# Performance work log

Hardware: AMD Instinct MI355X
Metric: run time of the kernel (lower is better)

## Reference

```python
import jax, jax.numpy as jnp
import numpy as np

HEAD = 12
HEAD_DIM = 64  # dim // head = 768 // 12


def setup_inputs() -> dict:
    key = jax.random.key(0)
    k1, k2, k3 = jax.random.split(key, 3)
    B, N, D = 4, 2048, 768
    scale = 1.0 / np.sqrt(D)
    return {
        "x": jax.random.normal(k1, (B, N, D), dtype=jnp.float32),
        "w_qkv": jax.random.normal(k2, (D, 3 * D), dtype=jnp.float32) * scale,
        "w_proj": jax.random.normal(k3, (D, D), dtype=jnp.float32) * scale,
        "b_proj": jnp.zeros((D,), dtype=jnp.float32),
    }


def reference(x, w_qkv, w_proj, b_proj):
    B, N, D = x.shape
    qkv = x @ w_qkv  # [B, N, 3D]
    q, k, v = jnp.split(qkv, 3, axis=-1)
    # [B, H, N, k]
    def heads(t):
        return t.reshape(B, N, HEAD, HEAD_DIM).transpose(0, 2, 1, 3)
    q, k, v = heads(q), heads(k), heads(v)
    attn = jnp.einsum("bhnd,bhmd->bhnm", q, k) / jnp.sqrt(jnp.float32(HEAD_DIM))
    attn_prob = jax.nn.softmax(attn, axis=-1)  # dropout p=0.0 -> identity
    out = jnp.einsum("bhnm,bhmd->bhnd", attn_prob, v)
    out = out.transpose(0, 2, 1, 3).reshape(B, N, D)
    return out @ w_proj + b_proj
```

## Files before the change

### kernel.cpp

```cpp
#include <hip/hip_runtime.h>

typedef unsigned short u16;
typedef unsigned int u32;
typedef u16 u16x4 __attribute__((ext_vector_type(4)));
typedef u16 u16x8 __attribute__((ext_vector_type(8)));
typedef u32 u32x2 __attribute__((ext_vector_type(2)));
typedef u32 u32x4 __attribute__((ext_vector_type(4)));
typedef __bf16 bf16x8 __attribute__((ext_vector_type(8)));
typedef float f32x4 __attribute__((ext_vector_type(4)));
typedef float f32x16 __attribute__((ext_vector_type(16)));

#define MFMA16 __builtin_amdgcn_mfma_f32_16x16x32_bf16
#define MFMA32 __builtin_amdgcn_mfma_f32_32x32x16_bf16

__device__ __forceinline__ u16 f2bf(float f) {
  return __builtin_bit_cast(u16, (__bf16)f);
}

__device__ __forceinline__ u32 pk2bf(float a, float b) {
  return (u32)__builtin_bit_cast(u16, (__bf16)a) |
         ((u32)__builtin_bit_cast(u16, (__bf16)b) << 16);
}

__device__ __forceinline__ u32x2 swap32(u32 a, u32 b, int hi) {
#if __has_builtin(__builtin_amdgcn_permlane32_swap)
  (void)hi;
  return __builtin_amdgcn_permlane32_swap(a, b, false, false);
#else
  u32 sa = (u32)__shfl_xor((int)a, 32), sb = (u32)__shfl_xor((int)b, 32);
  u32x2 r;
  r[0] = hi ? sb : a;
  r[1] = hi ? b : sa;
  return r;
#endif
}

__device__ __forceinline__ void gload_lds16(const void* g, void* l) {
  __builtin_amdgcn_global_load_lds(
      (const __attribute__((address_space(1))) u32*)g,
      (__attribute__((address_space(3))) u32*)l, 16, 0, 0);
}

__global__ __launch_bounds__(256)
void prepass_kernel(const float* __restrict__ x, u16* __restrict__ xb,
                    const float* __restrict__ wq, u16* __restrict__ wqT,
                    const float* __restrict__ wp, u16* __restrict__ wpT) {
  __shared__ float t[32][33];
  const int bid = blockIdx.x, tid = threadIdx.x;
  if (bid < 6144) {
    const int i = bid * 256 + tid;
    float4 v = reinterpret_cast<const float4*>(x)[i];
    u16x4 o;
    o[0] = f2bf(v.x); o[1] = f2bf(v.y); o[2] = f2bf(v.z); o[3] = f2bf(v.w);
    reinterpret_cast<u16x4*>(xb)[i] = o;
    return;
  }
  const float* w;
  u16* wt;
  int N, b2;
  if (bid < 7872) { b2 = bid - 6144; w = wq; wt = wqT; N = 2304; }
  else            { b2 = bid - 7872; w = wp; wt = wpT; N = 768; }
  const int K = 768;
  const int bk = (b2 % 24) * 32, bn = (b2 / 24) * 32;
  const int xx = tid & 31, yy = tid >> 5;
#pragma unroll
  for (int j = 0; j < 32; j += 8)
    t[yy + j][xx] = w[(size_t)(bk + yy + j) * N + bn + xx];
  __syncthreads();
#pragma unroll
  for (int j = 0; j < 32; j += 8)
    wt[(size_t)(bn + yy + j) * K + bk + xx] = f2bf(t[xx][yy + j]);
}

#define QSCALE 0.18033688011112042f

template <int NTOT, int EPI, int NT>
__global__ __launch_bounds__(256)
void gemm_bf16_kernel(const u16* __restrict__ A, const u16* __restrict__ BT,
                      u16* __restrict__ qo, u16* __restrict__ ko,
                      u16* __restrict__ vt, float* __restrict__ outF,
                      const float* __restrict__ bias) {
  __shared__ u16 sh[16384];
  u16* As = sh;
  u16* Bs = sh + 8192;
  const int tid = threadIdx.x;
  const int l = tid & 63, w = tid >> 6;
  const int lr = l & 15, lg = l >> 4;
  const int swz = (blockIdx.x & 7) * (8 * NT) + (blockIdx.x >> 3);
  const int mtile = swz / NT;
  const int ntile = swz % NT;
  const int mbase = mtile * 128, nbase = ntile * 128;
  const int wr = (w >> 1) * 64, wc = (w & 1) * 64;

  f32x4 acc[4][4] = {};

  for (int k0 = 0; k0 < 768; k0 += 64) {
#pragma unroll
    for (int i = 0; i < 4; ++i) {
      const int c = w * 64 + i * 256 + l;
      const int row = c >> 3, c16 = c & 7;
      const int sc = c16 ^ (row & 7);
      gload_lds16(A + (size_t)(mbase + row) * 768 + k0 + sc * 8,
                  &As[(size_t)(w * 64 + i * 256) * 8]);
      gload_lds16(BT + (size_t)(nbase + row) * 768 + k0 + sc * 8,
                  &Bs[(size_t)(w * 64 + i * 256) * 8]);
    }
    __syncthreads();
#pragma unroll
    for (int ks = 0; ks < 2; ++ks) {
      bf16x8 af[4], bfr[4];
#pragma unroll
      for (int m = 0; m < 4; ++m) {
        const int row = wr + m * 16 + lr;
        const int byte = (row * 128 + ks * 64 + lg * 16) ^ ((row & 7) << 4);
        af[m] = *reinterpret_cast<const bf16x8*>((const char*)As + byte);
      }
#pragma unroll
      for (int n = 0; n < 4; ++n) {
        const int row = wc + n * 16 + lr;
        const int byte = (row * 128 + ks * 64 + lg * 16) ^ ((row & 7) << 4);
        bfr[n] = *reinterpret_cast<const bf16x8*>((const char*)Bs + byte);
      }
#pragma unroll
      for (int m = 0; m < 4; ++m)
#pragma unroll
        for (int n = 0; n < 4; ++n)
          acc[m][n] = MFMA16(af[m], bfr[n], acc[m][n], 0, 0, 0);
    }
    __syncthreads();
  }

  if (EPI == 0 && ntile >= 12) {
    u16* vts = sh;
#pragma unroll
    for (int m = 0; m < 4; ++m)
#pragma unroll
      for (int n = 0; n < 4; ++n)
#pragma unroll
        for (int r = 0; r < 4; ++r) {
          const int col = wc + n * 16 + lr;
          const int row = wr + m * 16 + lg * 4 + r;
          const int byte = col * 256 + ((row * 2) ^ ((col & 7) << 4));
          *reinterpret_cast<u16*>((char*)vts + byte) = f2bf(acc[m][n][r]);
        }
    __syncthreads();
    const int b2 = mbase >> 11, nn0 = mbase & 2047;
#pragma unroll
    for (int i = 0; i < 8; ++i) {
      const int idx = i * 256 + tid;
      const int col = idx >> 4, u = idx & 15;
      u16x8 vv = *reinterpret_cast<u16x8*>(
          (char*)vts + (col * 256 + ((u * 16) ^ ((col & 7) << 4))));
      const int cg = nbase - 1536 + col;
      const int hh = cg >> 6, dd = cg & 63;
      *reinterpret_cast<u16x8*>(
          vt + (((size_t)(b2 * 12 + hh)) * 64 + dd) * 2048 + nn0 + u * 8) = vv;
    }
    return;
  }

#pragma unroll
  for (int m = 0; m < 4; ++m) {
#pragma unroll
    for (int n = 0; n < 4; ++n) {
#pragma unroll
      for (int r = 0; r < 4; ++r) {
        const int row = mbase + wr + m * 16 + lg * 4 + r;
        const int col = nbase + wc + n * 16 + lr;
        float val = acc[m][n][r];
        if (EPI == 0) {
          const int w2 = col / 768;
          const int c2 = col - w2 * 768;
          const int hh = c2 >> 6, dd = c2 & 63;
          const int b2 = row >> 11, nn = row & 2047;
          u16* dst = (w2 == 0) ? qo : ko;
          if (w2 == 0) val *= QSCALE;
          dst[(((size_t)(b2 * 12 + hh)) * 2048 + nn) * 64 + dd] = f2bf(val);
        } else {
          outF[(size_t)row * NTOT + col] = val + bias[col];
        }
      }
    }
  }
}

__global__ __launch_bounds__(256)
void flash_attn32_kernel(const u16* __restrict__ qb, const u16* __restrict__ kb,
                         const u16* __restrict__ vtb, u16* __restrict__ ao) {
  __shared__ u16 sh[32768];
  const int tid = threadIdx.x, w = tid >> 6, l = tid & 63;
  const int q5 = l & 31, hi = l >> 5;
  const int swz = (blockIdx.x & 7) * 96 + (blockIdx.x >> 3);
  const int bh = swz >> 4, qt = swz & 15;
  const int b = bh / 12, h = bh % 12;
  const int qrow0 = qt * 128 + w * 32;
  const u16* Q = qb + ((size_t)bh * 2048 + qrow0) * 64;
  const u16* K = kb + (size_t)bh * 2048 * 64;
  const u16* Vg = vtb + (size_t)bh * 64 * 2048;

  bf16x8 qf[4];
#pragma unroll
  for (int dk = 0; dk < 4; ++dk)
    qf[dk] = *reinterpret_cast<const bf16x8*>(Q + (size_t)q5 * 64 + dk * 16 + hi * 8);

  f32x16 ot0 = {}, ot1 = {};
  float l_ = 0.f;

  auto stage2 = [&](u16* base, int kt0) {
#pragma unroll
    for (int s = 0; s < 2; ++s) {
      u16* sb = base + s * 8192;
      const int kt = kt0 + s * 64;
#pragma unroll
      for (int i = 0; i < 2; ++i) {
        const int c = w * 64 + i * 256 + l;
        const int L = c >> 4, C = (c & 15) ^ (L & 15);
        const int row = L + ((C >> 3) << 5);
        gload_lds16(K + (size_t)(kt + row) * 64 + (C & 7) * 8,
                    sb + (size_t)(w * 64 + i * 256) * 8);
      }
#pragma unroll
      for (int i = 0; i < 2; ++i) {
        const int c = w * 64 + i * 256 + l;
        const int L = c >> 4, C = (c & 15) ^ (L & 15);
        const int d = L + ((C >> 3) << 5);
        gload_lds16(Vg + (size_t)d * 2048 + kt + (C & 7) * 8,
                    sb + 4096 + (size_t)(w * 64 + i * 256) * 8);
      }
    }
  };

  stage2(sh, 0);
  int cur = 0;
  const int q15 = q5 & 15;

  for (int win = 0; win < 16; ++win) {
    u16* tb = sh + cur * 16384;
    __builtin_amdgcn_sched_barrier(0);
    __builtin_amdgcn_s_barrier();
    __builtin_amdgcn_sched_barrier(0);
    if (win + 1 < 16) {
      stage2(sh + (cur ^ 1) * 16384, (win + 1) * 128);
      asm volatile("s_waitcnt vmcnt(8)" ::: "memory");
    } else {
      asm volatile("s_waitcnt vmcnt(0)" ::: "memory");
    }
    __builtin_amdgcn_sched_barrier(0);
    __builtin_amdgcn_s_barrier();
    __builtin_amdgcn_sched_barrier(0);

    const char* ksbA = (const char*)tb;
    const char* vsbA = (const char*)(tb + 4096);
    const char* ksbB = (const char*)(tb + 8192);
    const char* vsbB = (const char*)(tb + 12288);

    f32x16 sA0 = {}, sA1 = {}, sB0 = {}, sB1 = {};
    __builtin_amdgcn_s_setprio(1);
#pragma unroll
    for (int dk = 0; dk < 4; ++dk) {
      const int C = dk * 2 + hi;
      const int o0 = (C ^ q15) << 4, o1 = (((C + 8) ^ q15)) << 4;
      bf16x8 ka0 = *reinterpret_cast<const bf16x8*>(ksbA + q5 * 256 + o0);
      bf16x8 ka1 = *reinterpret_cast<const bf16x8*>(ksbA + q5 * 256 + o1);
      bf16x8 kb0 = *reinterpret_cast<const bf16x8*>(ksbB + q5 * 256 + o0);
      bf16x8 kb1 = *reinterpret_cast<const bf16x8*>(ksbB + q5 * 256 + o1);
      sA0 = MFMA32(ka0, qf[dk], sA0, 0, 0, 0);
      sA1 = MFMA32(ka1, qf[dk], sA1, 0, 0, 0);
      sB0 = MFMA32(kb0, qf[dk], sB0, 0, 0, 0);
      sB1 = MFMA32(kb1, qf[dk], sB1, 0, 0, 0);
    }
    __builtin_amdgcn_s_setprio(0);

    float p0 = 0.f, p1 = 0.f, p2 = 0.f, p3 = 0.f;
#pragma unroll
    for (int r = 0; r < 16; ++r) {
      sA0[r] = __builtin_amdgcn_exp2f(sA0[r]);
      if (r & 1) p1 += sA0[r]; else p0 += sA0[r];
    }
#pragma unroll
    for (int r = 0; r < 16; ++r) {
      sA1[r] = __builtin_amdgcn_exp2f(sA1[r]);
      if (r & 1) p3 += sA1[r]; else p2 += sA1[r];
    }
    l_ += (p0 + p1) + (p2 + p3);
    float p4 = 0.f, p5 = 0.f, p6 = 0.f, p7 = 0.f;
#pragma unroll
    for (int r = 0; r < 16; ++r) {
      sB0[r] = __builtin_amdgcn_exp2f(sB0[r]);
      if (r & 1) p5 += sB0[r]; else p4 += sB0[r];
    }
#pragma unroll
    for (int r = 0; r < 16; ++r) {
      sB1[r] = __builtin_amdgcn_exp2f(sB1[r]);
      if (r & 1) p7 += sB1[r]; else p6 += sB1[r];
    }
    l_ += (p4 + p5) + (p6 + p7);

    __builtin_amdgcn_s_setprio(1);
#pragma unroll
    for (int kvs = 0; kvs < 4; ++kvs) {
      const f32x16& stx = (kvs < 2) ? sA0 : sA1;
      const int rb = (kvs & 1) * 8;
      const u32 A0 = pk2bf(stx[rb + 0], stx[rb + 1]);
      const u32 A1 = pk2bf(stx[rb + 2], stx[rb + 3]);
      const u32 A2 = pk2bf(stx[rb + 4], stx[rb + 5]);
      const u32 A3 = pk2bf(stx[rb + 6], stx[rb + 7]);
      const u32x2 p02 = swap32(A0, A2, hi);
      const u32x2 p13 = swap32(A1, A3, hi);
      u32x4 wv;
      wv[0] = p02[0]; wv[1] = p13[0]; wv[2] = p02[1]; wv[3] = p13[1];
      const bf16x8 pf = __builtin_bit_cast(bf16x8, wv);
      const int Cv = kvs * 2 + hi;
      bf16x8 vf0 = *reinterpret_cast<const bf16x8*>(
          vsbA + q5 * 256 + ((Cv ^ q15) << 4));
      bf16x8 vf1 = *reinterpret_cast<const bf16x8*>(
          vsbA + q5 * 256 + (((Cv + 8) ^ q15) << 4));
      ot0 = MFMA32(vf0, pf, ot0, 0, 0, 0);
      ot1 = MFMA32(vf1, pf, ot1, 0, 0, 0);
    }
#pragma unroll
    for (int kvs = 0; kvs < 4; ++kvs) {
      const f32x16& stx = (kvs < 2) ? sB0 : sB1;
      const int rb = (kvs & 1) * 8;
      const u32 A0 = pk2bf(stx[rb + 0], stx[rb + 1]);
      const u32 A1 = pk2bf(stx[rb + 2], stx[rb + 3]);
      const u32 A2 = pk2bf(stx[rb + 4], stx[rb + 5]);
      const u32 A3 = pk2bf(stx[rb + 6], stx[rb + 7]);
      const u32x2 p02 = swap32(A0, A2, hi);
      const u32x2 p13 = swap32(A1, A3, hi);
      u32x4 wv;
      wv[0] = p02[0]; wv[1] = p13[0]; wv[2] = p02[1]; wv[3] = p13[1];
      const bf16x8 pf = __builtin_bit_cast(bf16x8, wv);
      const int Cv = kvs * 2 + hi;
      bf16x8 vf0 = *reinterpret_cast<const bf16x8*>(
          vsbB + q5 * 256 + ((Cv ^ q15) << 4));
      bf16x8 vf1 = *reinterpret_cast<const bf16x8*>(
          vsbB + q5 * 256 + (((Cv + 8) ^ q15) << 4));
      ot0 = MFMA32(vf0, pf, ot0, 0, 0, 0);
      ot1 = MFMA32(vf1, pf, ot1, 0, 0, 0);
    }
    __builtin_amdgcn_s_setprio(0);
    cur ^= 1;
  }

  l_ += __shfl_xor(l_, 32);

  u16* ob = sh + w * 2048;
  const float inv = 1.0f / l_;
  const int swo = (q5 & 7) << 4;
#pragma unroll
  for (int g = 0; g < 4; ++g) {
    u16x4 pk0, pk1;
#pragma unroll
    for (int r = 0; r < 4; ++r) {
      pk0[r] = f2bf(ot0[g * 4 + r] * inv);
      pk1[r] = f2bf(ot1[g * 4 + r] * inv);
    }
    const int d0 = hi * 4 + g * 8;
    *reinterpret_cast<u16x4*>((char*)ob + ((q5 * 128 + d0 * 2) ^ swo)) = pk0;
    *reinterpret_cast<u16x4*>((char*)ob + ((q5 * 128 + (d0 + 32) * 2) ^ swo)) = pk1;
  }
  __syncthreads();
#pragma unroll
  for (int i = 0; i < 4; ++i) {
    const int idx = i * 64 + l;
    const int qr = idx >> 3, cc = idx & 7;
    u16x8 vv = *reinterpret_cast<u16x8*>(
        (char*)ob + ((qr * 128 + cc * 16) ^ ((qr & 7) << 4)));
    *reinterpret_cast<u16x8*>(
        ao + ((size_t)(b * 2048 + qrow0 + qr)) * 768 + h * 64 + cc * 8) = vv;
  }
}

extern "C" void kernel_launch(void* const* d_in, const int* in_sizes, int n_in,
                              void* d_out, int out_size, void* d_ws,
                              size_t ws_size, hipStream_t stream) {
  const float* x = (const float*)d_in[0];
  const float* w_qkv = (const float*)d_in[1];
  const float* w_proj = (const float*)d_in[2];
  const float* b_proj = (const float*)d_in[3];
  float* out = (float*)d_out;

  char* ws = (char*)d_ws;
  size_t off = 0;
  auto alloc = [&](size_t bytes) {
    char* p = ws + off;
    off += (bytes + 255) & ~(size_t)255;
    return p;
  };
  u16* xb = (u16*)alloc(8192ull * 768 * 2);
  u16* wqkvT = (u16*)alloc(2304ull * 768 * 2);
  u16* wprojT = (u16*)alloc(768ull * 768 * 2);
  u16* qbuf = (u16*)alloc(48ull * 2048 * 64 * 2);
  u16* kbuf = (u16*)alloc(48ull * 2048 * 64 * 2);
  u16* vtb = (u16*)alloc(48ull * 64 * 2048 * 2);
  u16* aob = (u16*)alloc(8192ull * 768 * 2);
  (void)ws_size; (void)n_in; (void)in_sizes; (void)out_size;

  prepass_kernel<<<8448, 256, 0, stream>>>(x, xb, w_qkv, wqkvT, w_proj, wprojT);

  gemm_bf16_kernel<2304, 0, 18><<<64 * 18, 256, 0, stream>>>(
      xb, wqkvT, qbuf, kbuf, vtb, nullptr, nullptr);

  flash_attn32_kernel<<<768, 256, 0, stream>>>(qbuf, kbuf, vtb, aob);

  gemm_bf16_kernel<768, 1, 6><<<64 * 6, 256, 0, stream>>>(
      aob, wprojT, nullptr, nullptr, nullptr, out, b_proj);
}
```

Measured before the change: 149.4 us.

## Process two 32-row query tiles per wave to reuse staged K/V tiles

Each wave now handles 64 query rows (two 32-row Q fragments) instead of 32, so a block covers 256 query rows and the grid halves to 384 blocks. Every K/V tile staged into shared memory is reused by twice as many MFMAs, which halves global K/V traffic and the barrier/staging overhead per unit of work. The cost is more registers (two sets of output accumulators and Q fragments), which may lower occupancy. With 384 blocks on a 256-CU part there is also a partial second wave of blocks, which risks load imbalance.

```diff
diff --git a/kernel.cpp b/kernel.cpp
--- a/kernel.cpp
+++ b/kernel.cpp
@@ -190,21 +190,24 @@
   __shared__ u16 sh[32768];
   const int tid = threadIdx.x, w = tid >> 6, l = tid & 63;
   const int q5 = l & 31, hi = l >> 5;
-  const int swz = (blockIdx.x & 7) * 96 + (blockIdx.x >> 3);
-  const int bh = swz >> 4, qt = swz & 15;
+  const int swz = (blockIdx.x & 7) * 48 + (blockIdx.x >> 3);
+  const int bh = swz >> 3, qt = swz & 7;
   const int b = bh / 12, h = bh % 12;
-  const int qrow0 = qt * 128 + w * 32;
-  const u16* Q = qb + ((size_t)bh * 2048 + qrow0) * 64;
+  const int qrow0 = qt * 256 + w * 64;
+  const u16* QA = qb + ((size_t)bh * 2048 + qrow0) * 64;
+  const u16* QB = QA + 32 * 64;
   const u16* K = kb + (size_t)bh * 2048 * 64;
   const u16* Vg = vtb + (size_t)bh * 64 * 2048;
 
-  bf16x8 qf[4];
-#pragma unroll
-  for (int dk = 0; dk < 4; ++dk)
-    qf[dk] = *reinterpret_cast<const bf16x8*>(Q + (size_t)q5 * 64 + dk * 16 + hi * 8);
-
-  f32x16 ot0 = {}, ot1 = {};
-  float l_ = 0.f;
+  bf16x8 qfA[4], qfB[4];
+#pragma unroll
+  for (int dk = 0; dk < 4; ++dk) {
+    qfA[dk] = *reinterpret_cast<const bf16x8*>(QA + (size_t)q5 * 64 + dk * 16 + hi * 8);
+    qfB[dk] = *reinterpret_cast<const bf16x8*>(QB + (size_t)q5 * 64 + dk * 16 + hi * 8);
+  }
+
+  f32x16 o0A = {}, o1A = {}, o0B = {}, o1B = {};
+  float lA = 0.f, lB = 0.f;
 
   auto stage2 = [&](u16* base, int kt0) {
 #pragma unroll
@@ -254,121 +257,147 @@
     const char* ksbB = (const char*)(tb + 8192);
     const char* vsbB = (const char*)(tb + 12288);
 
-    f32x16 sA0 = {}, sA1 = {}, sB0 = {}, sB1 = {};
-    __builtin_amdgcn_s_setprio(1);
-#pragma unroll
-    for (int dk = 0; dk < 4; ++dk) {
-      const int C = dk * 2 + hi;
-      const int o0 = (C ^ q15) << 4, o1 = (((C + 8) ^ q15)) << 4;
-      bf16x8 ka0 = *reinterpret_cast<const bf16x8*>(ksbA + q5 * 256 + o0);
-      bf16x8 ka1 = *reinterpret_cast<const bf16x8*>(ksbA + q5 * 256 + o1);
-      bf16x8 kb0 = *reinterpret_cast<const bf16x8*>(ksbB + q5 * 256 + o0);
-      bf16x8 kb1 = *reinterpret_cast<const bf16x8*>(ksbB + q5 * 256 + o1);
-      sA0 = MFMA32(ka0, qf[dk], sA0, 0, 0, 0);
-      sA1 = MFMA32(ka1, qf[dk], sA1, 0, 0, 0);
-      sB0 = MFMA32(kb0, qf[dk], sB0, 0, 0, 0);
-      sB1 = MFMA32(kb1, qf[dk], sB1, 0, 0, 0);
-    }
-    __builtin_amdgcn_s_setprio(0);
-
-    float p0 = 0.f, p1 = 0.f, p2 = 0.f, p3 = 0.f;
-#pragma unroll
-    for (int r = 0; r < 16; ++r) {
-      sA0[r] = __builtin_amdgcn_exp2f(sA0[r]);
-      if (r & 1) p1 += sA0[r]; else p0 += sA0[r];
-    }
-#pragma unroll
-    for (int r = 0; r < 16; ++r) {
-      sA1[r] = __builtin_amdgcn_exp2f(sA1[r]);
-      if (r & 1) p3 += sA1[r]; else p2 += sA1[r];
-    }
-    l_ += (p0 + p1) + (p2 + p3);
-    float p4 = 0.f, p5 = 0.f, p6 = 0.f, p7 = 0.f;
-#pragma unroll
-    for (int r = 0; r < 16; ++r) {
-      sB0[r] = __builtin_amdgcn_exp2f(sB0[r]);
-      if (r & 1) p5 += sB0[r]; else p4 += sB0[r];
-    }
-#pragma unroll
-    for (int r = 0; r < 16; ++r) {
-      sB1[r] = __builtin_amdgcn_exp2f(sB1[r]);
-      if (r & 1) p7 += sB1[r]; else p6 += sB1[r];
-    }
-    l_ += (p4 + p5) + (p6 + p7);
-
-    __builtin_amdgcn_s_setprio(1);
-#pragma unroll
-    for (int kvs = 0; kvs < 4; ++kvs) {
-      const f32x16& stx = (kvs < 2) ? sA0 : sA1;
-      const int rb = (kvs & 1) * 8;
-      const u32 A0 = pk2bf(stx[rb + 0], stx[rb + 1]);
-      const u32 A1 = pk2bf(stx[rb + 2], stx[rb + 3]);
-      const u32 A2 = pk2bf(stx[rb + 4], stx[rb + 5]);
-      const u32 A3 = pk2bf(stx[rb + 6], stx[rb + 7]);
-      const u32x2 p02 = swap32(A0, A2, hi);
-      const u32x2 p13 = swap32(A1, A3, hi);
-      u32x4 wv;
-      wv[0] = p02[0]; wv[1] = p13[0]; wv[2] = p02[1]; wv[3] = p13[1];
-      const bf16x8 pf = __builtin_bit_cast(bf16x8, wv);
-      const int Cv = kvs * 2 + hi;
-      bf16x8 vf0 = *reinterpret_cast<const bf16x8*>(
-          vsbA + q5 * 256 + ((Cv ^ q15) << 4));
-      bf16x8 vf1 = *reinterpret_cast<const bf16x8*>(
-          vsbA + q5 * 256 + (((Cv + 8) ^ q15) << 4));
-      ot0 = MFMA32(vf0, pf, ot0, 0, 0, 0);
-      ot1 = MFMA32(vf1, pf, ot1, 0, 0, 0);
-    }
-#pragma unroll
-    for (int kvs = 0; kvs < 4; ++kvs) {
-      const f32x16& stx = (kvs < 2) ? sB0 : sB1;
-      const int rb = (kvs & 1) * 8;
-      const u32 A0 = pk2bf(stx[rb + 0], stx[rb + 1]);
-      const u32 A1 = pk2bf(stx[rb + 2], stx[rb + 3]);
-      const u32 A2 = pk2bf(stx[rb + 4], stx[rb + 5]);
-      const u32 A3 = pk2bf(stx[rb + 6], stx[rb + 7]);
-      const u32x2 p02 = swap32(A0, A2, hi);
-      const u32x2 p13 = swap32(A1, A3, hi);
-      u32x4 wv;
-      wv[0] = p02[0]; wv[1] = p13[0]; wv[2] = p02[1]; wv[3] = p13[1];
-      const bf16x8 pf = __builtin_bit_cast(bf16x8, wv);
-      const int Cv = kvs * 2 + hi;
-      bf16x8 vf0 = *reinterpret_cast<const bf16x8*>(
-          vsbB + q5 * 256 + ((Cv ^ q15) << 4));
-      bf16x8 vf1 = *reinterpret_cast<const bf16x8*>(
-          vsbB + q5 * 256 + (((Cv + 8) ^ q15) << 4));
-      ot0 = MFMA32(vf0, pf, ot0, 0, 0, 0);
-      ot1 = MFMA32(vf1, pf, ot1, 0, 0, 0);
-    }
-    __builtin_amdgcn_s_setprio(0);
+    auto compute = [&](const bf16x8* qf, f32x16& ot0, f32x16& ot1, float& l_) {
+      f32x16 sA0 = {}, sA1 = {}, sB0 = {}, sB1 = {};
+      __builtin_amdgcn_s_setprio(1);
+#pragma unroll
+      for (int dk = 0; dk < 4; ++dk) {
+        const int C = dk * 2 + hi;
+        const int o0 = (C ^ q15) << 4, o1 = (((C + 8) ^ q15)) << 4;
+        bf16x8 ka0 = *reinterpret_cast<const bf16x8*>(ksbA + q5 * 256 + o0);
+        bf16x8 ka1 = *reinterpret_cast<const bf16x8*>(ksbA + q5 * 256 + o1);
+        bf16x8 kb0 = *reinterpret_cast<const bf16x8*>(ksbB + q5 * 256 + o0);
+        bf16x8 kb1 = *reinterpret_cast<const bf16x8*>(ksbB + q5 * 256 + o1);
+        sA0 = MFMA32(ka0, qf[dk], sA0, 0, 0, 0);
+        sA1 = MFMA32(ka1, qf[dk], sA1, 0, 0, 0);
+        sB0 = MFMA32(kb0, qf[dk], sB0, 0, 0, 0);
+        sB1 = MFMA32(kb1, qf[dk], sB1, 0, 0, 0);
+      }
+      __builtin_amdgcn_s_setprio(0);
+
+      float p0 = 0.f, p1 = 0.f, p2 = 0.f, p3 = 0.f;
+#pragma unroll
+      for (int r = 0; r < 16; ++r) {
+        sA0[r] = __builtin_amdgcn_exp2f(sA0[r]);
+        if (r & 1) p1 += sA0[r]; else p0 += sA0[r];
+      }
+#pragma unroll
+      for (int r = 0; r < 16; ++r) {
+        sA1[r] = __builtin_amdgcn_exp2f(sA1[r]);
+        if (r & 1) p3 += sA1[r]; else p2 += sA1[r];
+      }
+      l_ += (p0 + p1) + (p2 + p3);
+      float p4 = 0.f, p5 = 0.f, p6 = 0.f, p7 = 0.f;
+#pragma unroll
+      for (int r = 0; r < 16; ++r) {
+        sB0[r] = __builtin_amdgcn_exp2f(sB0[r]);
+        if (r & 1) p5 += sB0[r]; else p4 += sB0[r];
+      }
+#pragma unroll
+      for (int r = 0; r < 16; ++r) {
+        sB1[r] = __builtin_amdgcn_exp2f(sB1[r]);
+        if (r & 1) p7 += sB1[r]; else p6 += sB1[r];
+      }
+      l_ += (p4 + p5) + (p6 + p7);
+
+      __builtin_amdgcn_s_setprio(1);
+#pragma unroll
+      for (int kvs = 0; kvs < 4; ++kvs) {
+        const f32x16& stx = (kvs < 2) ? sA0 : sA1;
+        const int rb = (kvs & 1) * 8;
+        const u32 A0 = pk2bf(stx[rb + 0], stx[rb + 1]);
+        const u32 A1 = pk2bf(stx[rb + 2], stx[rb + 3]);
+        const u32 A2 = pk2bf(stx[rb + 4], stx[rb + 5]);
+        const u32 A3 = pk2bf(stx[rb + 6], stx[rb + 7]);
+        const u32x2 p02 = swap32(A0, A2, hi);
+        const u32x2 p13 = swap32(A1, A3, hi);
+        u32x4 wv;
+        wv[0] = p02[0]; wv[1] = p13[0]; wv[2] = p02[1]; wv[3] = p13[1];
+        const bf16x8 pf = __builtin_bit_cast(bf16x8, wv);
+        const int Cv = kvs * 2 + hi;
+        bf16x8 vf0 = *reinterpret_cast<const bf16x8*>(
+            vsbA + q5 * 256 + ((Cv ^ q15) << 4));
+        bf16x8 vf1 = *reinterpret_cast<const bf16x8*>(
+            vsbA + q5 * 256 + (((Cv + 8) ^ q15) << 4));
+        ot0 = MFMA32(vf0, pf, ot0, 0, 0, 0);
+        ot1 = MFMA32(vf1, pf, ot1, 0, 0, 0);
+      }
+#pragma unroll
+      for (int kvs = 0; kvs < 4; ++kvs) {
+        const f32x16& stx = (kvs < 2) ? sB0 : sB1;
+        const int rb = (kvs & 1) * 8;
+        const u32 A0 = pk2bf(stx[rb + 0], stx[rb + 1]);
+        const u32 A1 = pk2bf(stx[rb + 2], stx[rb + 3]);
+        const u32 A2 = pk2bf(stx[rb + 4], stx[rb + 5]);
+        const u32 A3 = pk2bf(stx[rb + 6], stx[rb + 7]);
+        const u32x2 p02 = swap32(A0, A2, hi);
+        const u32x2 p13 = swap32(A1, A3, hi);
+        u32x4 wv;
+        wv[0] = p02[0]; wv[1] = p13[0]; wv[2] = p02[1]; wv[3] = p13[1];
+        const bf16x8 pf = __builtin_bit_cast(bf16x8, wv);
+        const int Cv = kvs * 2 + hi;
+        bf16x8 vf0 = *reinterpret_cast<const bf16x8*>(
+            vsbB + q5 * 256 + ((Cv ^ q15) << 4));
+        bf16x8 vf1 = *reinterpret_cast<const bf16x8*>(
+            vsbB + q5 * 256 + (((Cv + 8) ^ q15) << 4));
+        ot0 = MFMA32(vf0, pf, ot0, 0, 0, 0);
+        ot1 = MFMA32(vf1, pf, ot1, 0, 0, 0);
+      }
+      __builtin_amdgcn_s_setprio(0);
+    };
+
+    compute(qfA, o0A, o1A, lA);
+    compute(qfB, o0B, o1B, lB);
     cur ^= 1;
   }
 
-  l_ += __shfl_xor(l_, 32);
-
-  u16* ob = sh + w * 2048;
-  const float inv = 1.0f / l_;
+  lA += __shfl_xor(lA, 32);
+  lB += __shfl_xor(lB, 32);
+
   const int swo = (q5 & 7) << 4;
-#pragma unroll
-  for (int g = 0; g < 4; ++g) {
-    u16x4 pk0, pk1;
-#pragma unroll
-    for (int r = 0; r < 4; ++r) {
-      pk0[r] = f2bf(ot0[g * 4 + r] * inv);
-      pk1[r] = f2bf(ot1[g * 4 + r] * inv);
-    }
-    const int d0 = hi * 4 + g * 8;
-    *reinterpret_cast<u16x4*>((char*)ob + ((q5 * 128 + d0 * 2) ^ swo)) = pk0;
-    *reinterpret_cast<u16x4*>((char*)ob + ((q5 * 128 + (d0 + 32) * 2) ^ swo)) = pk1;
+  {
+    u16* ob = sh + (2 * w) * 2048;
+    const float inv = 1.0f / lA;
+#pragma unroll
+    for (int g = 0; g < 4; ++g) {
+      u16x4 pk0, pk1;
+#pragma unroll
+      for (int r = 0; r < 4; ++r) {
+        pk0[r] = f2bf(o0A[g * 4 + r] * inv);
+        pk1[r] = f2bf(o1A[g * 4 + r] * inv);
+      }
+      const int d0 = hi * 4 + g * 8;
+      *reinterpret_cast<u16x4*>((char*)ob + ((q5 * 128 + d0 * 2) ^ swo)) = pk0;
+      *reinterpret_cast<u16x4*>((char*)ob + ((q5 * 128 + (d0 + 32) * 2) ^ swo)) = pk1;
+    }
+  }
+  {
+    u16* ob = sh + (2 * w + 1) * 2048;
+    const float inv = 1.0f / lB;
+#pragma unroll
+    for (int g = 0; g < 4; ++g) {
+      u16x4 pk0, pk1;
+#pragma unroll
+      for (int r = 0; r < 4; ++r) {
+        pk0[r] = f2bf(o0B[g * 4 + r] * inv);
+        pk1[r] = f2bf(o1B[g * 4 + r] * inv);
+      }
+      const int d0 = hi * 4 + g * 8;
+      *reinterpret_cast<u16x4*>((char*)ob + ((q5 * 128 + d0 * 2) ^ swo)) = pk0;
+      *reinterpret_cast<u16x4*>((char*)ob + ((q5 * 128 + (d0 + 32) * 2) ^ swo)) = pk1;
+    }
   }
   __syncthreads();
 #pragma unroll
-  for (int i = 0; i < 4; ++i) {
-    const int idx = i * 64 + l;
+  for (int i = 0; i < 8; ++i) {
+    const int idx = i * 256 + tid;
     const int qr = idx >> 3, cc = idx & 7;
+    u16* rb = sh + (qr >> 5) * 2048;
+    const int q5r = qr & 31;
     u16x8 vv = *reinterpret_cast<u16x8*>(
-        (char*)ob + ((qr * 128 + cc * 16) ^ ((qr & 7) << 4)));
+        (char*)rb + ((q5r * 128 + cc * 16) ^ ((q5r & 7) << 4)));
     *reinterpret_cast<u16x8*>(
-        ao + ((size_t)(b * 2048 + qrow0 + qr)) * 768 + h * 64 + cc * 8) = vv;
+        ao + ((size_t)(b * 2048 + qt * 256 + qr)) * 768 + h * 64 + cc * 8) = vv;
   }
 }
 
@@ -402,7 +431,7 @@
   gemm_bf16_kernel<2304, 0, 18><<<64 * 18, 256, 0, stream>>>(
       xb, wqkvT, qbuf, kbuf, vtb, nullptr, nullptr);
 
-  flash_attn32_kernel<<<768, 256, 0, stream>>>(qbuf, kbuf, vtb, aob);
+  flash_attn32_kernel<<<384, 256, 0, stream>>>(qbuf, kbuf, vtb, aob);
 
   gemm_bf16_kernel<768, 1, 6><<<64 * 6, 256, 0, stream>>>(
       aob, wprojT, nullptr, nullptr, nullptr, out, b_proj);
```

Measured after the change: 175.1 us. +17.2%, slower.
